# Kernel optimization log

Hardware: AMD Instinct MI355X
Metric: run time of the kernel (lower is better)

## Reference

```python
import math
import jax, jax.numpy as jnp
import numpy as np

BATCH, SEQ, EMBED, HEADS = 2, 2048, 1024, 16
HEAD_DIM = EMBED // HEADS


def setup_inputs() -> dict:
    key = jax.random.key(0)
    k1, k2, k3 = jax.random.split(key, 3)
    scale = 1.0 / math.sqrt(EMBED)  # keep pre-softmax logits in a sane range
    x = jax.random.normal(k1, (BATCH, SEQ, EMBED), dtype=jnp.float32)
    mask = jnp.ones((BATCH, SEQ), dtype=jnp.int32)
    qkv_w = jax.random.normal(k2, (3 * EMBED, EMBED), dtype=jnp.float32) * scale
    out_w = jax.random.normal(k3, (EMBED, EMBED), dtype=jnp.float32) * scale
    out_b = jnp.zeros((EMBED,), dtype=jnp.float32)
    return {"x": x, "mask": mask, "qkv_w": qkv_w, "out_w": out_w, "out_b": out_b}


def reference(x, mask, qkv_w, out_w, out_b):
    b, s, e = x.shape
    # qkv projection (torch Linear: x @ W.T), then split heads
    qkv = (x @ qkv_w.T).reshape(b, s, 3, HEADS, HEAD_DIM)
    q, k, v = qkv[:, :, 0], qkv[:, :, 1], qkv[:, :, 2]  # each [b,s,h,d]
    # full score matrix [b,h,s,s]
    scores = jnp.einsum('bshd,bthd->bhst', q, k) / math.sqrt(HEAD_DIM)
    # mask broadcast over query dim and heads: [b,1,1,s_keys]
    scores = jnp.where(mask[:, None, None, :] == 0, -jnp.inf, scores)
    attn = jax.nn.softmax(scores, axis=-1)
    # dropout is identity in eval mode
    out = jnp.einsum('bhst,bthd->bshd', attn, v).reshape(b, s, e)
    return out @ out_w.T + out_b
```

## Files before the change

kernel.cpp:

```cpp
#include <hip/hip_runtime.h>
#include <hip/hip_bf16.h>

#define BATCH 2
#define SEQ   2048
#define EMBED 1024
#define HEADS 16
#define HDIM  64
#define NBH   (BATCH*HEADS)

typedef __attribute__((ext_vector_type(8))) short short8;
typedef __attribute__((ext_vector_type(4))) float floatx4;
typedef unsigned short u16;
typedef unsigned int   u32;

#define LOG2E 1.4426950408889634f

__device__ __forceinline__ void async_cp16(const void* g, void* l) {
  __builtin_amdgcn_global_load_lds((const __attribute__((address_space(1))) void*)g,
                                   (__attribute__((address_space(3))) void*)l,
                                   16, 0, 0);
}

__device__ __forceinline__ u16 f2b(float f) {
  union { float f; u32 u; } x; x.f = f;
  return (u16)((x.u + 0x7fffu + ((x.u >> 16) & 1u)) >> 16);
}
__device__ __forceinline__ u32 pk2(float a, float b) {
  __hip_bfloat162 t = __float22bfloat162_rn(make_float2(a, b));
  return *reinterpret_cast<u32*>(&t);
}
__device__ __forceinline__ float fexp2(float x) {
#if __has_builtin(__builtin_amdgcn_exp2f)
  return __builtin_amdgcn_exp2f(x);
#else
  return __expf(x * 0.6931471805599453f);
#endif
}

__global__ __launch_bounds__(256)
void cvt_all(const float* __restrict__ x, const float* __restrict__ wqkv,
             const float* __restrict__ wo,
             u16* __restrict__ xb, u16* __restrict__ wqkvb, u16* __restrict__ wob) {
  const size_t t = (size_t)blockIdx.x * 256 + threadIdx.x;
  const float* src; u16* dst; size_t off;
  if (t < 1048576) { src = x; dst = xb; off = t; }
  else if (t < 1048576 + 786432) { src = wqkv; dst = wqkvb; off = t - 1048576; }
  else { src = wo; dst = wob; off = t - (1048576 + 786432); }
  float4 v = *(const float4*)(src + off * 4);
  ushort4 o;
  o.x = f2b(v.x); o.y = f2b(v.y); o.z = f2b(v.z); o.w = f2b(v.w);
  *(ushort4*)(dst + off * 4) = o;
}

__global__ __launch_bounds__(256, 3)
void qkv_gemm(const u16* __restrict__ X, const u16* __restrict__ W,
              u16* __restrict__ q_ws, u16* __restrict__ k_ws,
              u16* __restrict__ vT_ws) {
  __shared__ u16 As[8][128][8];
  __shared__ u16 Bs[8][128][8];
  const int tid  = threadIdx.x;
  const int lane = tid & 63, wv = tid >> 6;
  const int l15  = lane & 15, quad = lane >> 4;
  const int wm = (wv >> 1) << 6, wn = (wv & 1) << 6;
  const int m0 = blockIdx.y << 7, n0 = blockIdx.x << 7;
  const bool vpath = (n0 >= 2048);

  floatx4 acc[4][4];
#pragma unroll
  for (int i = 0; i < 4; ++i)
#pragma unroll
    for (int j = 0; j < 4; ++j) acc[i][j] = {0.f, 0.f, 0.f, 0.f};

  if (!vpath) {
    for (int k0 = 0; k0 < EMBED; k0 += 64) {
      __syncthreads();
#pragma unroll
      for (int i = 0; i < 4; ++i) {
        int c = tid + (i << 8);
        int kb = c >> 7, row = c & 127;
        async_cp16(X + (size_t)(m0 + row) * EMBED + k0 + kb * 8, &As[kb][row][0]);
        async_cp16(W + (size_t)(n0 + row) * EMBED + k0 + kb * 8, &Bs[kb][row][0]);
      }
      __syncthreads();

#pragma unroll
      for (int ks = 0; ks < 2; ++ks) {
        short8 af[4], bf[4];
#pragma unroll
        for (int t = 0; t < 4; ++t) {
          af[t] = *(const short8*)&As[ks * 4 + quad][wm + t * 16 + l15][0];
          bf[t] = *(const short8*)&Bs[ks * 4 + quad][wn + t * 16 + l15][0];
        }
#pragma unroll
        for (int i = 0; i < 4; ++i)
#pragma unroll
          for (int j = 0; j < 4; ++j)
            acc[i][j] = __builtin_amdgcn_mfma_f32_16x16x32_bf16(bf[j], af[i], acc[i][j], 0, 0, 0);
      }
    }

#pragma unroll
    for (int i = 0; i < 4; ++i) {
      int mg = m0 + wm + i * 16 + l15;
      int b = mg >> 11, s = mg & 2047;
#pragma unroll
      for (int j = 0; j < 4; ++j) {
        int col0 = n0 + wn + j * 16 + (quad << 2);
        int c = col0 >> 10, hd = col0 & 1023;
        int h = hd >> 6, d0 = hd & 63;
        u16* dst = c ? k_ws : q_ws;
        uint2 w;
        w.x = pk2(acc[i][j][0], acc[i][j][1]);
        w.y = pk2(acc[i][j][2], acc[i][j][3]);
        *(uint2*)(dst + (((size_t)(b * HEADS + h)) * SEQ + s) * HDIM + d0) = w;
      }
    }
  } else {
    for (int k0 = 0; k0 < EMBED; k0 += 64) {
      __syncthreads();
#pragma unroll
      for (int i = 0; i < 4; ++i) {
        int c = tid + (i << 8);
        int kb = c >> 7, row = c & 127;
        async_cp16(X + (size_t)(m0 + row) * EMBED + k0 + kb * 8, &As[kb][row][0]);
        async_cp16(W + (size_t)(n0 + row) * EMBED + k0 + kb * 8, &Bs[kb][row][0]);
      }
      __syncthreads();

#pragma unroll
      for (int ks = 0; ks < 2; ++ks) {
        short8 af[4], bf[4];
#pragma unroll
        for (int t = 0; t < 4; ++t) {
          af[t] = *(const short8*)&As[ks * 4 + quad][wm + t * 16 + l15][0];
          bf[t] = *(const short8*)&Bs[ks * 4 + quad][wn + t * 16 + l15][0];
        }
#pragma unroll
        for (int i = 0; i < 4; ++i)
#pragma unroll
          for (int j = 0; j < 4; ++j)
            acc[i][j] = __builtin_amdgcn_mfma_f32_16x16x32_bf16(af[i], bf[j], acc[i][j], 0, 0, 0);
      }
    }

#pragma unroll
    for (int i = 0; i < 4; ++i) {
      int mg0 = m0 + wm + i * 16 + (quad << 2);
      int b = mg0 >> 11, s0 = mg0 & 2047;
#pragma unroll
      for (int j = 0; j < 4; ++j) {
        int col = n0 + wn + j * 16 + l15;
        int hd = col & 1023;
        int h = hd >> 6, d = hd & 63;
        uint2 w;
        w.x = pk2(acc[i][j][0], acc[i][j][1]);
        w.y = pk2(acc[i][j][2], acc[i][j][3]);
        *(uint2*)(vT_ws + (((size_t)(b * HEADS + h)) * HDIM + d) * SEQ + s0) = w;
      }
    }
  }
}

__global__ __launch_bounds__(256, 4)
void attn_kernel(const u16* __restrict__ q_ws, const u16* __restrict__ k_ws,
                 const u16* __restrict__ vT_ws, const int* __restrict__ mask,
                 u16* __restrict__ ao) {
  __shared__ u16 Ks[8][64][8];
  __shared__ u16 Vt[8][64][8];
  __shared__ u16 Ps[4][16][68];
  __shared__ float msk[64];

  const int tid  = threadIdx.x;
  const int lane = tid & 63, wv = tid >> 6;
  const int l15  = lane & 15, quad = lane >> 4;
  const int bh = blockIdx.y;
  const int b  = bh >> 4, h = bh & 15;
  const int qrw = (blockIdx.x << 6) + (wv << 4);

  const u16* Qb  = q_ws  + (size_t)bh * SEQ * HDIM;
  const u16* Kb  = k_ws  + (size_t)bh * SEQ * HDIM;
  const u16* VbT = vT_ws + (size_t)bh * HDIM * SEQ;

  short8 qf[2];
#pragma unroll
  for (int s = 0; s < 2; ++s) {
    short8 v = *(const short8*)(Qb + (size_t)(qrw + l15) * HDIM + s * 32 + quad * 8);
#pragma unroll
    for (int e = 0; e < 8; ++e) {
      union { float f; u32 u; } x;
      x.u = ((u32)(u16)v[e]) << 16;
      x.f *= 0.125f;
      v[e] = (short)(x.u >> 16);
    }
    qf[s] = v;
  }

  float l_acc = 0.f;
  floatx4 O[4];
#pragma unroll
  for (int dt = 0; dt < 4; ++dt) O[dt] = {0.f, 0.f, 0.f, 0.f};

  for (int t0 = 0; t0 < SEQ; t0 += 64) {
    __syncthreads();
#pragma unroll
    for (int i = 0; i < 2; ++i) {
      int c = tid + (i << 8);
      int kb = c >> 6, r = c & 63;
      async_cp16(Kb + (size_t)(t0 + r) * HDIM + kb * 8, &Ks[kb][r][0]);
      async_cp16(VbT + (size_t)r * SEQ + t0 + kb * 8, &Vt[kb][r][0]);
    }
    if (tid < 64) msk[tid] = mask[b * SEQ + t0 + tid] ? -12.0f : -1e30f;
    __syncthreads();

    floatx4 sc[4];
#pragma unroll
    for (int nt = 0; nt < 4; ++nt) {
      sc[nt] = {0.f, 0.f, 0.f, 0.f};
#pragma unroll
      for (int s = 0; s < 2; ++s) {
        short8 kf = *(const short8*)&Ks[s * 4 + quad][nt * 16 + l15][0];
        sc[nt] = __builtin_amdgcn_mfma_f32_16x16x32_bf16(kf, qf[s], sc[nt], 0, 0, 0);
      }
    }

#pragma unroll
    for (int nt = 0; nt < 4; ++nt) {
      const float4 m4 = *(const float4*)&msk[nt * 16 + quad * 4];
      float pv[4];
#pragma unroll
      for (int r = 0; r < 4; ++r) {
        pv[r] = fexp2(fmaf(sc[nt][r], LOG2E, (&m4.x)[r]));
        l_acc += pv[r];
      }
      uint2 w;
      w.x = pk2(pv[0], pv[1]); w.y = pk2(pv[2], pv[3]);
      *(uint2*)&Ps[wv][l15][nt * 16 + (quad << 2)] = w;
    }

#pragma unroll
    for (int tch = 0; tch < 2; ++tch) {
      short8 pf = *(const short8*)&Ps[wv][l15][tch * 32 + quad * 8];
#pragma unroll
      for (int dt = 0; dt < 4; ++dt) {
        short8 vf = *(const short8*)&Vt[tch * 4 + quad][dt * 16 + l15][0];
        O[dt] = __builtin_amdgcn_mfma_f32_16x16x32_bf16(vf, pf, O[dt], 0, 0, 0);
      }
    }
  }

  l_acc += __shfl_xor(l_acc, 16);
  l_acc += __shfl_xor(l_acc, 32);
  const float inv = 1.f / l_acc;

  const size_t rowbase = ((size_t)(b * SEQ + qrw + l15)) * EMBED + h * 64;
#pragma unroll
  for (int dt = 0; dt < 4; ++dt) {
    uint2 w;
    w.x = pk2(O[dt][0] * inv, O[dt][1] * inv);
    w.y = pk2(O[dt][2] * inv, O[dt][3] * inv);
    *(uint2*)(ao + rowbase + dt * 16 + (quad << 2)) = w;
  }
}

__global__ __launch_bounds__(256, 2)
void proj_gemm(const u16* __restrict__ A, const u16* __restrict__ W,
               const float* __restrict__ bias, float* __restrict__ out) {
  __shared__ u16 As[4][128][8];
  __shared__ u16 Bs[4][64][8];
  const int tid  = threadIdx.x;
  const int lane = tid & 63, wv = tid >> 6;
  const int l15  = lane & 15, quad = lane >> 4;
  const int wm = (wv >> 1) << 6, wn = (wv & 1) << 5;
  const int m0 = blockIdx.y << 7, n0 = blockIdx.x << 6;

  floatx4 acc[4][2];
#pragma unroll
  for (int i = 0; i < 4; ++i)
#pragma unroll
    for (int j = 0; j < 2; ++j) acc[i][j] = {0.f, 0.f, 0.f, 0.f};

  for (int k0 = 0; k0 < EMBED; k0 += 32) {
    __syncthreads();
#pragma unroll
    for (int i = 0; i < 2; ++i) {
      int c = tid + (i << 8);
      int kb = c >> 7, row = c & 127;
      async_cp16(A + (size_t)(m0 + row) * EMBED + k0 + kb * 8, &As[kb][row][0]);
    }
    {
      int kb = tid >> 6, row = tid & 63;
      async_cp16(W + (size_t)(n0 + row) * EMBED + k0 + kb * 8, &Bs[kb][row][0]);
    }
    __syncthreads();

    short8 af[4], bf[2];
#pragma unroll
    for (int t = 0; t < 4; ++t)
      af[t] = *(const short8*)&As[quad][wm + t * 16 + l15][0];
#pragma unroll
    for (int t = 0; t < 2; ++t)
      bf[t] = *(const short8*)&Bs[quad][wn + t * 16 + l15][0];
#pragma unroll
    for (int i = 0; i < 4; ++i)
#pragma unroll
      for (int j = 0; j < 2; ++j)
        acc[i][j] = __builtin_amdgcn_mfma_f32_16x16x32_bf16(bf[j], af[i], acc[i][j], 0, 0, 0);
  }

#pragma unroll
  for (int i = 0; i < 4; ++i) {
    int m = m0 + wm + i * 16 + l15;
#pragma unroll
    for (int j = 0; j < 2; ++j) {
      int col0 = n0 + wn + j * 16 + (quad << 2);
      float4 bv = *(const float4*)(bias + col0);
      float4 o;
      o.x = acc[i][j][0] + bv.x;
      o.y = acc[i][j][1] + bv.y;
      o.z = acc[i][j][2] + bv.z;
      o.w = acc[i][j][3] + bv.w;
      *(float4*)(out + (size_t)m * EMBED + col0) = o;
    }
  }
}

extern "C" void kernel_launch(void* const* d_in, const int* in_sizes, int n_in,
                              void* d_out, int out_size, void* d_ws, size_t ws_size,
                              hipStream_t stream) {
  const float* x     = (const float*)d_in[0];
  const int*   mask  = (const int*)d_in[1];
  const float* qkv_w = (const float*)d_in[2];
  const float* out_w = (const float*)d_in[3];
  const float* out_b = (const float*)d_in[4];
  float* out = (float*)d_out;

  const size_t per = (size_t)NBH * SEQ * HDIM;
  u16* xb    = (u16*)d_ws;
  u16* wqkvb = xb + 4194304;
  u16* wob   = wqkvb + 3145728;
  u16* q_ws  = wob + 1048576;
  u16* k_ws  = q_ws + per;
  u16* vT_ws = k_ws + per;
  u16* ao    = vT_ws + per;

  cvt_all<<<8192, 256, 0, stream>>>(x, qkv_w, out_w, xb, wqkvb, wob);
  qkv_gemm<<<dim3(24, 32), 256, 0, stream>>>(xb, wqkvb, q_ws, k_ws, vT_ws);
  attn_kernel<<<dim3(SEQ / 64, NBH), 256, 0, stream>>>(q_ws, k_ws, vT_ws, mask, ao);
  proj_gemm<<<dim3(16, 32), 256, 0, stream>>>(ao, wob, out_b, out);
}
```

Before: 240.7 us.

## Split attention key range across two blocks and combine partial outputs

Attention is split along the key dimension into two halves via a third grid dimension, so each block processes 1024 keys and twice as many blocks are launched. Unnormalized partial outputs are written in bf16 to reused workspace buffers along with per-row partial sums, and a new combine kernel adds them and normalizes. The intent is more parallelism and better occupancy (launch bounds raised to 6). In exchange it adds an extra kernel launch, extra global traffic for the partials, and bf16 rounding of unnormalized partials. It relies on a fixed softmax max offset rather than a running max, so the partials can be summed directly.

After: 262.1 us. 1.09x slower.

```diff
diff --git a/kernel.cpp b/kernel.cpp
--- a/kernel.cpp
+++ b/kernel.cpp
@@ -24,6 +24,10 @@
 __device__ __forceinline__ u16 f2b(float f) {
   union { float f; u32 u; } x; x.f = f;
   return (u16)((x.u + 0x7fffu + ((x.u >> 16) & 1u)) >> 16);
+}
+__device__ __forceinline__ float b2f(u16 b) {
+  union { float f; u32 u; } x; x.u = ((u32)b) << 16;
+  return x.f;
 }
 __device__ __forceinline__ u32 pk2(float a, float b) {
   __hip_bfloat162 t = __float22bfloat162_rn(make_float2(a, b));
@@ -161,10 +165,11 @@
   }
 }
 
-__global__ __launch_bounds__(256, 4)
-void attn_kernel(const u16* __restrict__ q_ws, const u16* __restrict__ k_ws,
-                 const u16* __restrict__ vT_ws, const int* __restrict__ mask,
-                 u16* __restrict__ ao) {
+__global__ __launch_bounds__(256, 6)
+void attn_part(const u16* __restrict__ q_ws, const u16* __restrict__ k_ws,
+               const u16* __restrict__ vT_ws, const int* __restrict__ mask,
+               u16* __restrict__ Opart0, u16* __restrict__ Opart1,
+               float* __restrict__ lpart) {
   __shared__ u16 Ks[8][64][8];
   __shared__ u16 Vt[8][64][8];
   __shared__ u16 Ps[4][16][68];
@@ -175,7 +180,9 @@
   const int l15  = lane & 15, quad = lane >> 4;
   const int bh = blockIdx.y;
   const int b  = bh >> 4, h = bh & 15;
+  const int z  = blockIdx.z;
   const int qrw = (blockIdx.x << 6) + (wv << 4);
+  const int tbase = z << 10;
 
   const u16* Qb  = q_ws  + (size_t)bh * SEQ * HDIM;
   const u16* Kb  = k_ws  + (size_t)bh * SEQ * HDIM;
@@ -200,7 +207,8 @@
 #pragma unroll
   for (int dt = 0; dt < 4; ++dt) O[dt] = {0.f, 0.f, 0.f, 0.f};
 
-  for (int t0 = 0; t0 < SEQ; t0 += 64) {
+  for (int ti = 0; ti < 16; ++ti) {
+    const int t0 = tbase + (ti << 6);
     __syncthreads();
 #pragma unroll
     for (int i = 0; i < 2; ++i) {
@@ -250,16 +258,39 @@
 
   l_acc += __shfl_xor(l_acc, 16);
   l_acc += __shfl_xor(l_acc, 32);
-  const float inv = 1.f / l_acc;
-
+  if (quad == 0)
+    lpart[((size_t)z << 16) + bh * SEQ + qrw + l15] = l_acc;
+
+  u16* Op = z ? Opart1 : Opart0;
   const size_t rowbase = ((size_t)(b * SEQ + qrw + l15)) * EMBED + h * 64;
 #pragma unroll
   for (int dt = 0; dt < 4; ++dt) {
     uint2 w;
-    w.x = pk2(O[dt][0] * inv, O[dt][1] * inv);
-    w.y = pk2(O[dt][2] * inv, O[dt][3] * inv);
-    *(uint2*)(ao + rowbase + dt * 16 + (quad << 2)) = w;
-  }
+    w.x = pk2(O[dt][0], O[dt][1]);
+    w.y = pk2(O[dt][2], O[dt][3]);
+    *(uint2*)(Op + rowbase + dt * 16 + (quad << 2)) = w;
+  }
+}
+
+__global__ __launch_bounds__(256)
+void attn_combine(u16* __restrict__ Opart0, const u16* __restrict__ Opart1,
+                  const float* __restrict__ lpart) {
+  const size_t idx4 = (size_t)blockIdx.x * 256 + threadIdx.x;
+  const size_t i = idx4 << 2;
+  const int b = (int)(i >> 21), s = (int)((i >> 10) & 2047), h = (int)((i >> 6) & 15);
+  const size_t lidx = (size_t)((b << 4) | h) * SEQ + s;
+  const float inv = 1.f / (lpart[lidx] + lpart[lidx + (1u << 16)]);
+
+  uint2 a = *(const uint2*)(Opart0 + i);
+  uint2 c = *(const uint2*)(Opart1 + i);
+  float o0 = b2f((u16)(a.x)) + b2f((u16)(c.x));
+  float o1 = b2f((u16)(a.x >> 16)) + b2f((u16)(c.x >> 16));
+  float o2 = b2f((u16)(a.y)) + b2f((u16)(c.y));
+  float o3 = b2f((u16)(a.y >> 16)) + b2f((u16)(c.y >> 16));
+  uint2 w;
+  w.x = pk2(o0 * inv, o1 * inv);
+  w.y = pk2(o2 * inv, o3 * inv);
+  *(uint2*)(Opart0 + i) = w;
 }
 
 __global__ __launch_bounds__(256, 2)
@@ -342,9 +373,13 @@
   u16* k_ws  = q_ws + per;
   u16* vT_ws = k_ws + per;
   u16* ao    = vT_ws + per;
+  u16* Opart0 = ao;
+  u16* Opart1 = xb;
+  float* lpart = (float*)wqkvb;
 
   cvt_all<<<8192, 256, 0, stream>>>(x, qkv_w, out_w, xb, wqkvb, wob);
   qkv_gemm<<<dim3(24, 32), 256, 0, stream>>>(xb, wqkvb, q_ws, k_ws, vT_ws);
-  attn_kernel<<<dim3(SEQ / 64, NBH), 256, 0, stream>>>(q_ws, k_ws, vT_ws, mask, ao);
+  attn_part<<<dim3(SEQ / 64, NBH, 2), 256, 0, stream>>>(q_ws, k_ws, vT_ws, mask, Opart0, Opart1, lpart);
+  attn_combine<<<4096, 256, 0, stream>>>(Opart0, Opart1, lpart);
   proj_gemm<<<dim3(16, 32), 256, 0, stream>>>(ao, wob, out_b, out);
 }
```
